# Kernel tuning notes

Hardware: AMD Instinct MI355X
Metric: run time of the kernel (lower is better)

Reference implementation:

```python
import jax, jax.numpy as jnp
import numpy as np

# static config (matches init_kwargs)
NH, NKV, E, K = 16, 4, 8, 2
CAP_FACTOR = 1.25
LN_EPS = 1e-5


def _layer_norm(x, w, b):
    mu = jnp.mean(x, axis=-1, keepdims=True)
    var = jnp.mean(jnp.square(x - mu), axis=-1, keepdims=True)
    return (x - mu) * jax.lax.rsqrt(var + LN_EPS) * w + b


def setup_inputs() -> dict:
    key = jax.random.key(0)
    ks = jax.random.split(key, 6)
    S, B, H, F = 2048, 1, 1024, 2048
    HD = H // NH
    qkv_out = NKV * ((NH // NKV) + 2) * HD  # 1536
    f32 = jnp.float32
    return {
        "hidden_states": jax.random.normal(ks[0], (S, B, H), f32),
        "ln1_weight": jnp.ones((H,), f32),
        "ln1_bias": jnp.zeros((H,), f32),
        "ln2_weight": jnp.ones((H,), f32),
        "ln2_bias": jnp.zeros((H,), f32),
        "qkv_weight": jax.random.normal(ks[1], (qkv_out, H), f32) * 0.02,
        "proj_weight": jax.random.normal(ks[2], (H, H), f32) * 0.02,
        "router_weight": jax.random.normal(ks[3], (H, E), f32) * 0.02,
        "moe_w1": jax.random.normal(ks[4], (E, H, F), f32) * 0.02,
        "moe_w2": jax.random.normal(ks[5], (F and E, F, H), f32)[:E] * 0.02 if False else jax.random.normal(ks[5], (E, F, H), f32) * 0.02,
    }


def reference(hidden_states, ln1_weight, ln1_bias, ln2_weight, ln2_bias,
              qkv_weight, proj_weight, router_weight, moe_w1, moe_w2):
    S, B, H = hidden_states.shape
    HD = H // NH
    q_per_kv = NH // NKV
    # ---- attention block (cp_size=1: all-to-alls are identity) ----
    ln1 = _layer_norm(hidden_states, ln1_weight, ln1_bias)
    qkv = jnp.einsum('sbh,oh->sbo', ln1, qkv_weight)
    qkv = qkv.reshape(S, B, NKV, (q_per_kv + 2) * HD)
    q = qkv[..., : q_per_kv * HD].reshape(S, B, NH, HD)
    k = qkv[..., q_per_kv * HD:(q_per_kv + 1) * HD]          # [S,B,NKV,HD]
    v = qkv[..., (q_per_kv + 1) * HD:]                        # [S,B,NKV,HD]
    qb = jnp.transpose(q, (1, 2, 0, 3)).reshape(B, NKV, q_per_kv, S, HD)
    kb = jnp.transpose(k, (1, 2, 0, 3))                       # [B,NKV,S,HD]
    vb = jnp.transpose(v, (1, 2, 0, 3))
    scale = 1.0 / np.sqrt(HD).astype(np.float32)
    scores = jnp.einsum('bgqsd,bgtd->bgqst', qb, kb) * scale  # [B,NKV,qpk,S,S]
    causal = jnp.tril(jnp.ones((S, S), bool))
    scores = jnp.where(causal, scores, jnp.finfo(scores.dtype).min)
    attn = jax.nn.softmax(scores, axis=-1)
    ao = jnp.einsum('bgqst,bgtd->bgqsd', attn, vb)
    ao = ao.reshape(B, NH, S, HD)
    ao = jnp.transpose(ao, (2, 0, 1, 3)).reshape(S, B, H)
    proj = jnp.einsum('sbh,oh->sbo', ao, proj_weight)
    h1 = hidden_states + proj
    # ---- MoE block (ep_size=1: uniform all-to-all is identity) ----
    ln2 = _layer_norm(h1, ln2_weight, ln2_bias)
    x = ln2.reshape(-1, H)                                    # [N,H]
    N = x.shape[0]
    logits = x @ router_weight                                # linear(x, router_weight.t())
    probs = jax.nn.softmax(logits, axis=-1)
    top_p, top_i = jax.lax.top_k(probs, K)
    top_p = top_p / jnp.sum(top_p, axis=-1, keepdims=True)
    exp_idx = top_i.reshape(-1)                               # [N*K]
    exp_p = top_p.reshape(-1)
    # stable sort by expert id, capacity-padded dispatch
    order = jnp.argsort(exp_idx, stable=True)
    sorted_exp = exp_idx[order]
    counts = jnp.bincount(exp_idx, length=E)
    offsets = jnp.concatenate([jnp.zeros((1,), counts.dtype), jnp.cumsum(counts)[:-1]])
    within = jnp.arange(N * K) - offsets[sorted_exp]
    cap = int(np.ceil(N * K / E * CAP_FACTOR))
    T = E * cap
    valid = within < cap
    dst = jnp.where(valid, sorted_exp * cap + within, T)      # T = out-of-bounds -> dropped
    padded_tokens = jnp.zeros((T, H), x.dtype).at[dst].set(x[order // K], mode='drop')
    padded_probs = jnp.zeros((T,), exp_p.dtype).at[dst].set(exp_p[order], mode='drop')
    padded_tid = jnp.zeros((T,), jnp.int32).at[dst].set((order // K).astype(jnp.int32), mode='drop')
    # grouped expert GEMMs: [E,cap,H] x [E,H,F] -> gelu -> [E,cap,H]
    xt = padded_tokens.reshape(E, cap, H)
    fc1 = jax.nn.gelu(jnp.einsum('ech,ehf->ecf', xt, moe_w1))
    fc2 = jnp.einsum('ecf,efh->ech', fc1, moe_w2).reshape(T, H)
    weighted = fc2 * padded_probs[:, None]                    # pad slots have prob 0
    moe_out = jnp.zeros((N, H), hidden_states.dtype).at[padded_tid].add(weighted)
    return h1 + moe_out.reshape(S, B, H)
```

## Files before the change

kernel.cpp:

```cpp
#include <hip/hip_runtime.h>
#include <hip/hip_bf16.h>
#include <stdint.h>

#define S_LEN 2048
#define HDIM  1024
#define NHEAD 16
#define NKVH  4
#define HEADD 64
#define QKV_O 1536
#define NEXP  8
#define TOPK  2
#define CAP   640
#define TCAP  (NEXP*CAP)
#define FDIM  2048
#define LOG2E 1.44269504088896f
#define NCHUNK 40
#define ATTN_BLOCKS (NCHUNK*NHEAD)
#define TRANSP_BLOCKS 4096

typedef __bf16 bf16x8 __attribute__((ext_vector_type(8)));
typedef float  f32x4  __attribute__((ext_vector_type(4)));
typedef unsigned int u32;
typedef u32 u32x4 __attribute__((ext_vector_type(4)));
typedef u32 u32x2 __attribute__((ext_vector_type(2)));
typedef unsigned short u16;
typedef u16 u16x8 __attribute__((ext_vector_type(8)));

__device__ __forceinline__ void gload16(const __bf16* g, __bf16* l) {
    __builtin_amdgcn_global_load_lds(
        (const __attribute__((address_space(1))) u32*)g,
        (__attribute__((address_space(3))) u32*)l, 16, 0, 0);
}

__device__ __constant__ const signed char c_strip[NCHUNK] =
    {0,1,2,3, 4,4, 5,5, 6,6, 7,7, 8,8,8, 9,9,9, 10,10,10, 11,11,11,
     12,12,12,12, 13,13,13,13, 14,14,14,14, 15,15,15,15};
__device__ __constant__ const signed char c_chunk[NCHUNK] =
    {0,0,0,0, 0,1, 0,1, 0,1, 0,1, 0,1,2, 0,1,2, 0,1,2, 0,1,2,
     0,1,2,3, 0,1,2,3, 0,1,2,3, 0,1,2,3};
__device__ __constant__ const signed char c_cbase[16] = {0,1,2,3,4,6,8,10,12,15,18,21,24,28,32,36};
__device__ __constant__ const signed char c_nch[16]   = {1,1,1,1,2,2,2,2,3,3,3,3,4,4,4,4};

__global__ __launch_bounds__(256)
void prep_kernel(const float* __restrict__ hidden, const float* __restrict__ ln1w,
                 const float* __restrict__ ln1bb, const float* __restrict__ qkvW,
                 const float* __restrict__ projW, __bf16* __restrict__ ln1o,
                 __bf16* __restrict__ projWb, __bf16* __restrict__ qkvWb) {
    const int b = blockIdx.x, tid = threadIdx.x;
    if (b < S_LEN) {
        __shared__ float red[256];
        const float* x = hidden + (size_t)b * HDIM;
        float xr[4];
        #pragma unroll
        for (int j = 0; j < 4; ++j) xr[j] = x[tid + 256*j];
        float s = xr[0] + xr[1] + xr[2] + xr[3];
        red[tid] = s; __syncthreads();
        for (int st = 128; st > 0; st >>= 1) { if (tid < st) red[tid] += red[tid+st]; __syncthreads(); }
        float mu = red[0] / HDIM; __syncthreads();
        float v = 0.f;
        #pragma unroll
        for (int j = 0; j < 4; ++j) { float d = xr[j]-mu; v += d*d; }
        red[tid] = v; __syncthreads();
        for (int st = 128; st > 0; st >>= 1) { if (tid < st) red[tid] += red[tid+st]; __syncthreads(); }
        float rstd = rsqrtf(red[0]/HDIM + 1e-5f);
        #pragma unroll
        for (int j = 0; j < 4; ++j) {
            int i = tid + 256*j;
            ln1o[(size_t)b*HDIM + i] = (__bf16)((xr[j]-mu)*rstd*ln1w[i] + ln1bb[i]);
        }
        return;
    }
    const float* src; __bf16* dst; int i;
    if (b < S_LEN + 768) { src = qkvW; dst = qkvWb; i = (b - S_LEN)*256 + tid; }
    else                 { src = projW; dst = projWb; i = (b - S_LEN - 768)*256 + tid; }
    const float4* s = (const float4*)src + (size_t)i*2;
    float4 a = s[0], b4 = s[1];
    __bf16 tmp[8] = {(__bf16)a.x,(__bf16)a.y,(__bf16)a.z,(__bf16)a.w,
                     (__bf16)b4.x,(__bf16)b4.y,(__bf16)b4.z,(__bf16)b4.w};
    *(u32x4*)(dst + (size_t)i*8) = *(u32x4*)tmp;
}

template<int EPI>
__global__ __launch_bounds__(256)
void gemm_bf16_kernel(const __bf16* __restrict__ A, const __bf16* __restrict__ Bt,
                      const float* __restrict__ R, void* __restrict__ Cout,
                      int N, int K, long sA, long sB, long sC) {
    __shared__ __bf16 As[128*64];
    __shared__ __bf16 Bs[128*64];
    const int e = blockIdx.z;
    A  += (size_t)e * sA;
    Bt += (size_t)e * sB;
    const int m0 = blockIdx.y*128, n0 = blockIdx.x*128;
    const int tid = threadIdx.x;
    const int lane = tid & 63, w = tid >> 6;
    const int lr = lane & 15, lg = lane >> 4;
    const int wr = w >> 1, wc = w & 1;
    const int srow8 = lane >> 3, sg = lane & 7;
    f32x4 acc[4][4] = {};
    for (int k0 = 0; k0 < K; k0 += 64) {
        __syncthreads();
        #pragma unroll
        for (int i = 0; i < 4; ++i) {
            int row = 32*w + 8*i + srow8;
            int src_g = sg ^ (row & 7);
            gload16(A  + (size_t)(m0+row)*K + k0 + src_g*8,
                    (__bf16*)((char*)As + (32*w + 8*i)*128));
            gload16(Bt + (size_t)(n0+row)*K + k0 + src_g*8,
                    (__bf16*)((char*)Bs + (32*w + 8*i)*128));
        }
        __syncthreads();
        #pragma unroll
        for (int ks = 0; ks < 2; ++ks) {
            bf16x8 af[4], bfr[4];
            #pragma unroll
            for (int mi = 0; mi < 4; ++mi) {
                int row = wr*64 + mi*16 + lr;
                af[mi] = *(const bf16x8*)((const char*)As + ((row*128 + (lg+4*ks)*16) ^ ((row&7)<<4)));
            }
            #pragma unroll
            for (int ni = 0; ni < 4; ++ni) {
                int row = wc*64 + ni*16 + lr;
                bfr[ni] = *(const bf16x8*)((const char*)Bs + ((row*128 + (lg+4*ks)*16) ^ ((row&7)<<4)));
            }
            #pragma unroll
            for (int mi = 0; mi < 4; ++mi)
                #pragma unroll
                for (int ni = 0; ni < 4; ++ni)
                    acc[mi][ni] = __builtin_amdgcn_mfma_f32_16x16x32_bf16(af[mi], bfr[ni], acc[mi][ni], 0,0,0);
        }
    }
    #pragma unroll
    for (int mi = 0; mi < 4; ++mi) {
        #pragma unroll
        for (int ni = 0; ni < 4; ++ni) {
            #pragma unroll
            for (int r = 0; r < 4; ++r) {
                int row = m0 + wr*64 + mi*16 + lg*4 + r;
                int col = n0 + wc*64 + ni*16 + lr;
                float v = acc[mi][ni][r];
                if (EPI == 1) v += R[(size_t)row*N + col];
                if (EPI == 2) {
                    float t = 0.7978845608028654f * (v + 0.044715f*v*v*v);
                    v = 0.5f * v * (1.f + tanhf(t));
                }
                if (EPI == 2 || EPI == 3)
                    ((__bf16*)Cout)[(size_t)e*sC + (size_t)row*N + col] = (__bf16)v;
                else
                    ((float*)Cout)[(size_t)e*sC + (size_t)row*N + col] = v;
            }
        }
    }
}

__global__ __launch_bounds__(512)
void attn_transp_kernel(const __bf16* __restrict__ qkv, float* __restrict__ partO,
                        float* __restrict__ partML,
                        const float* __restrict__ w1, const float* __restrict__ w2,
                        __bf16* __restrict__ w1t, __bf16* __restrict__ w2t) {
    __shared__ __attribute__((aligned(16))) char smem[49152];
    const int bid = blockIdx.x;

    if (bid >= ATTN_BLOCKS) {
        const int half = threadIdx.x >> 8, t256 = threadIdx.x & 255;
        float (*t)[65] = (float(*)[65])(smem + half*16640);
        const int tile = (bid - ATTN_BLOCKS)*2 + half;
        const float* src; __bf16* dst; int K, N, n0, k0;
        if (tile < 4096) {
            int e = tile >> 9, rem = tile & 511;
            K = HDIM; N = FDIM; n0 = (rem & 31) * 64; k0 = (rem >> 5) * 64;
            src = w1 + (size_t)e*K*N; dst = w1t + (size_t)e*K*N;
        } else {
            int tt = tile - 4096; int e = tt >> 9, rem = tt & 511;
            K = FDIM; N = HDIM; n0 = (rem & 15) * 64; k0 = (rem >> 4) * 64;
            src = w2 + (size_t)e*K*N; dst = w2t + (size_t)e*K*N;
        }
        const int r = t256 >> 4, c4 = (t256 & 15) * 4;
        #pragma unroll
        for (int i = 0; i < 4; ++i) {
            float4 v = *(const float4*)(src + (size_t)(k0 + r + 16*i)*N + n0 + c4);
            t[r+16*i][c4+0] = v.x; t[r+16*i][c4+1] = v.y;
            t[r+16*i][c4+2] = v.z; t[r+16*i][c4+3] = v.w;
        }
        __syncthreads();
        const int rn = t256 >> 3, kc = (t256 & 7) * 8;
        #pragma unroll
        for (int i = 0; i < 2; ++i) {
            int n = rn + 32*i;
            __bf16 tmp[8];
            #pragma unroll
            for (int j = 0; j < 8; ++j) tmp[j] = (__bf16)t[kc+j][n];
            *(u32x4*)(dst + (size_t)(n0+n)*K + k0 + kc) = *(u32x4*)tmp;
        }
        return;
    }

    __bf16* Kls = (__bf16*)smem;
    __bf16* Vls = (__bf16*)(smem + 16384);
    const int cx = bid % NCHUNK;
    const int h  = bid / NCHUNK;
    const int hg = h >> 2, qi = h & 3;
    const int qb = c_strip[cx];
    const int t0 = 4 * c_chunk[cx];
    const int t1 = min(qb + 1, t0 + 4);
    const int q0 = qb * 128;
    const int tid  = threadIdx.x;
    const int w    = tid >> 6;
    const int lane = tid & 63;
    const int lr   = lane & 15;
    const int lg   = lane >> 4;

    const int krow = tid >> 2, kc = (tid & 3) * 2;
    const int va = tid & 63,  dg  = tid >> 6;
    u32x4 kreg[2]; u16x8 vreg[2];

    const __bf16* kbase = qkv + hg*384 + 256;
    const __bf16* vbase = qkv + hg*384 + 320;

#define ISSUE(T) do { \
        const __bf16* kp = kbase + (size_t)((T)*128 + krow)*QKV_O + kc*8; \
        kreg[0] = *(const u32x4*)(kp); \
        kreg[1] = *(const u32x4*)(kp + 8); \
        const __bf16* vp = vbase + (size_t)((T)*128 + 2*va)*QKV_O + dg*8; \
        vreg[0] = *(const u16x8*)(vp); \
        vreg[1] = *(const u16x8*)(vp + QKV_O); \
    } while(0)

#define COMMIT() do { \
        char* Kb = (char*)Kls; \
        *(u32x4*)(Kb + ((krow*128 + (kc+0)*16) ^ ((krow&7)<<4))) = kreg[0]; \
        *(u32x4*)(Kb + ((krow*128 + (kc+1)*16) ^ ((krow&7)<<4))) = kreg[1]; \
        char* Vb = (char*)Vls; \
        _Pragma("unroll") \
        for (int j = 0; j < 8; ++j) { \
            int d = dg*8 + j; \
            u32 u = ((u32)vreg[1][j] << 16) | vreg[0][j]; \
            *(u32*)(Vb + ((d*256 + va*4) ^ ((d&7)<<4))) = u; \
        } \
    } while(0)

    const int qrow = q0 + w*16 + lr;
    const __bf16* qp = qkv + (size_t)qrow*QKV_O + hg*384 + qi*64;
    bf16x8 qfrag[2];
    #pragma unroll
    for (int ks = 0; ks < 2; ++ks) {
        bf16x8 qr = *(const bf16x8*)(qp + ks*32 + lg*8);
        #pragma unroll
        for (int j = 0; j < 8; ++j) qfrag[ks][j] = (__bf16)((float)qr[j] * 0.125f);
    }
    bf16x8 ones;
    #pragma unroll
    for (int j = 0; j < 8; ++j) ones[j] = (__bf16)1.0f;

    f32x4 oacc[4] = {};
    f32x4 lcol = {};
    float mrow[4] = {-INFINITY,-INFINITY,-INFINITY,-INFINITY};

    ISSUE(t0);
    for (int t = t0; t < t1; ++t) {
        __syncthreads();
        COMMIT();
        if (t+1 < t1) ISSUE(t+1);
        __syncthreads();

        f32x4 sacc[8] = {};
        const char* Kb = (const char*)Kls;
        #pragma unroll
        for (int f = 0; f < 8; ++f) {
            int row = lr + 16*f;
            int swz = (row & 7) << 4;
            #pragma unroll
            for (int ks = 0; ks < 2; ++ks) {
                bf16x8 kf = *(const bf16x8*)(Kb + ((row*128 + (lg*8+32*ks)*2) ^ swz));
                sacc[f] = __builtin_amdgcn_mfma_f32_16x16x32_bf16(qfrag[ks], kf, sacc[f], 0,0,0);
            }
        }
        if (t == qb) {
            #pragma unroll
            for (int f = 0; f < 8; ++f)
                #pragma unroll
                for (int r = 0; r < 4; ++r)
                    if (lr + 16*f > 16*w + 4*lg + r) sacc[f][r] = -INFINITY;
        }
        float tm[4];
        #pragma unroll
        for (int r = 0; r < 4; ++r) {
            float a = fmaxf(fmaxf(sacc[0][r], sacc[1][r]), fmaxf(sacc[2][r], sacc[3][r]));
            float b2 = fmaxf(fmaxf(sacc[4][r], sacc[5][r]), fmaxf(sacc[6][r], sacc[7][r]));
            tm[r] = fmaxf(a, b2);
        }
        #pragma unroll
        for (int msk = 1; msk < 16; msk <<= 1)
            #pragma unroll
            for (int r = 0; r < 4; ++r) tm[r] = fmaxf(tm[r], __shfl_xor(tm[r], msk, 64));
        float corr[4];
        #pragma unroll
        for (int r = 0; r < 4; ++r) {
            float mn = fmaxf(mrow[r], tm[r]);
            corr[r] = exp2f((mrow[r]-mn)*LOG2E);
            mrow[r] = mn;
        }
        #pragma unroll
        for (int f = 0; f < 8; ++f)
            #pragma unroll
            for (int r = 0; r < 4; ++r)
                sacc[f][r] = exp2f((sacc[f][r]-mrow[r])*LOG2E);
        #pragma unroll
        for (int ct = 0; ct < 4; ++ct)
            #pragma unroll
            for (int r = 0; r < 4; ++r) oacc[ct][r] *= corr[r];
        #pragma unroll
        for (int r = 0; r < 4; ++r) lcol[r] *= corr[r];

        char* Pw = smem + 32768 + w*2048;
        const char* Vb = (const char*)Vls;
        #pragma unroll
        for (int half = 0; half < 2; ++half) {
            #pragma unroll
            for (int f = 0; f < 4; ++f)
                #pragma unroll
                for (int r = 0; r < 4; ++r) {
                    int row = 4*lg + r, col = lr + 16*f;
                    *(__bf16*)(Pw + ((row*128 + col*2) ^ ((row&7)<<4))) = (__bf16)sacc[4*half+f][r];
                }
            bf16x8 pa[2];
            #pragma unroll
            for (int ks = 0; ks < 2; ++ks)
                pa[ks] = *(const bf16x8*)(Pw + ((lr*128 + (lg*8+32*ks)*2) ^ ((lr&7)<<4)));
            #pragma unroll
            for (int ks = 0; ks < 2; ++ks)
                lcol = __builtin_amdgcn_mfma_f32_16x16x32_bf16(pa[ks], ones, lcol, 0,0,0);
            #pragma unroll
            for (int ct = 0; ct < 4; ++ct) {
                int row = lr + 16*ct;
                int swz = (row & 7) << 4;
                #pragma unroll
                for (int ks = 0; ks < 2; ++ks) {
                    int gks = 2*half + ks;
                    bf16x8 vf = *(const bf16x8*)(Vb + ((row*256 + (lg*8+32*gks)*2) ^ swz));
                    oacc[ct] = __builtin_amdgcn_mfma_f32_16x16x32_bf16(pa[ks], vf, oacc[ct], 0,0,0);
                }
            }
        }
    }
    const int p = h*NCHUNK + cx;
    float* po = partO + (size_t)p * (128*64);
    #pragma unroll
    for (int ct = 0; ct < 4; ++ct)
        #pragma unroll
        for (int r = 0; r < 4; ++r)
            po[(16*w + 4*lg + r)*64 + 16*ct + lr] = oacc[ct][r];
    if (lr == 0) {
        float* pm = partML + (size_t)p * 256;
        #pragma unroll
        for (int r = 0; r < 4; ++r) {
            pm[(16*w + 4*lg + r)*2    ] = mrow[r];
            pm[(16*w + 4*lg + r)*2 + 1] = lcol[r];
        }
    }
#undef ISSUE
#undef COMMIT
}

__global__ __launch_bounds__(256)
void attn_combine_kernel(const float* __restrict__ partO, const float* __restrict__ partML,
                         __bf16* __restrict__ ao) {
    const int rb = blockIdx.x, h = blockIdx.y;
    const int row0 = rb*8;
    const int qb = row0 >> 7;
    const int nc = c_nch[qb], cb = c_cbase[qb];
    const int tid = threadIdx.x;
    const int rl = tid >> 5, d2 = (tid & 31) * 2;
    const int grow = row0 + rl;
    const int srow = grow & 127;
    const int pbase = h*NCHUNK + cb;
    float mv[4], lv[4];
    float M = -INFINITY;
    for (int c = 0; c < nc; ++c) {
        const float* pm = partML + (size_t)(pbase+c)*256 + srow*2;
        mv[c] = pm[0]; lv[c] = pm[1];
        M = fmaxf(M, mv[c]);
    }
    float L = 0.f, a0 = 0.f, a1 = 0.f;
    for (int c = 0; c < nc; ++c) {
        float wc = exp2f((mv[c]-M)*LOG2E);
        L += wc * lv[c];
        const float* po = partO + (size_t)(pbase+c)*(128*64) + srow*64 + d2;
        a0 += wc * po[0];
        a1 += wc * po[1];
    }
    float inv = 1.f / L;
    __bf16 o2[2] = {(__bf16)(a0*inv), (__bf16)(a1*inv)};
    *(u32*)(ao + (size_t)grow*HDIM + h*64 + d2) = *(u32*)o2;
}

__global__ __launch_bounds__(256)
void ln2_router_kernel(const float* __restrict__ h1, const float* __restrict__ w,
                       const float* __restrict__ b, const float* __restrict__ rw,
                       __bf16* __restrict__ x2b, int* __restrict__ expi,
                       float* __restrict__ expp) {
    const int t = blockIdx.x, tid = threadIdx.x;
    __shared__ float red[256];
    __shared__ float red8[256][8];
    const float* x = h1 + (size_t)t*HDIM;
    float xr[4];
    #pragma unroll
    for (int j = 0; j < 4; ++j) xr[j] = x[tid + 256*j];
    float s = xr[0] + xr[1] + xr[2] + xr[3];
    red[tid] = s; __syncthreads();
    for (int st = 128; st > 0; st >>= 1) { if (tid < st) red[tid] += red[tid+st]; __syncthreads(); }
    float mu = red[0] / HDIM; __syncthreads();
    float v = 0.f;
    #pragma unroll
    for (int j = 0; j < 4; ++j) { float d = xr[j]-mu; v += d*d; }
    red[tid] = v; __syncthreads();
    for (int st = 128; st > 0; st >>= 1) { if (tid < st) red[tid] += red[tid+st]; __syncthreads(); }
    float rstd = rsqrtf(red[0]/HDIM + 1e-5f);
    float part[8] = {};
    #pragma unroll
    for (int j = 0; j < 4; ++j) {
        int i = tid + 256*j;
        float o = (xr[j]-mu)*rstd*w[i] + b[i];
        x2b[(size_t)t*HDIM + i] = (__bf16)o;
        const float* wp = rw + (size_t)i*NEXP;
        #pragma unroll
        for (int e2 = 0; e2 < 8; ++e2) part[e2] += o * wp[e2];
    }
    #pragma unroll
    for (int e2 = 0; e2 < 8; ++e2) red8[tid][e2] = part[e2];
    __syncthreads();
    for (int st = 128; st > 0; st >>= 1) {
        if (tid < st)
            #pragma unroll
            for (int e2 = 0; e2 < 8; ++e2) red8[tid][e2] += red8[tid+st][e2];
        __syncthreads();
    }
    if (tid == 0) {
        float lg[8];
        #pragma unroll
        for (int e2 = 0; e2 < 8; ++e2) lg[e2] = red8[0][e2];
        int i0 = 0;
        for (int e2 = 1; e2 < 8; ++e2) if (lg[e2] > lg[i0]) i0 = e2;
        int i1 = -1;
        for (int e2 = 0; e2 < 8; ++e2) { if (e2 == i0) continue; if (i1 < 0 || lg[e2] > lg[i1]) i1 = e2; }
        float p1 = __expf(lg[i1] - lg[i0]);
        float inv = 1.f / (1.f + p1);
        expi[t*2]   = i0; expi[t*2+1] = i1;
        expp[t*2]   = inv; expp[t*2+1] = p1 * inv;
    }
}

__global__ __launch_bounds__(256)
void dst_fast_kernel(const int* __restrict__ expi, int* __restrict__ dst) {
    __shared__ int hist[256][9];
    const int tid = threadIdx.x;
    int ev[16];
    #pragma unroll
    for (int i = 0; i < 16; i += 4)
        *(int4*)(ev+i) = *(const int4*)(expi + tid*16 + i);
    int cnt[8] = {};
    #pragma unroll
    for (int i = 0; i < 16; ++i)
        #pragma unroll
        for (int e = 0; e < 8; ++e) cnt[e] += (ev[i] == e);
    #pragma unroll
    for (int e = 0; e < 8; ++e) hist[tid][e] = cnt[e];
    __syncthreads();
    const int w = tid >> 6, lane = tid & 63;
    #pragma unroll
    for (int rep = 0; rep < 2; ++rep) {
        int e = w + rep*4;
        int h0 = hist[4*lane+0][e], h1 = hist[4*lane+1][e],
            h2 = hist[4*lane+2][e], h3 = hist[4*lane+3][e];
        int s = h0+h1+h2+h3, inc = s;
        #pragma unroll
        for (int off = 1; off < 64; off <<= 1) {
            int v = __shfl_up(inc, off, 64);
            if (lane >= off) inc += v;
        }
        int excl = inc - s;
        hist[4*lane+0][e] = excl;
        hist[4*lane+1][e] = excl + h0;
        hist[4*lane+2][e] = excl + h0 + h1;
        hist[4*lane+3][e] = excl + h0 + h1 + h2;
    }
    __syncthreads();
    int run[8];
    #pragma unroll
    for (int e = 0; e < 8; ++e) run[e] = hist[tid][e];
    int out[16];
    #pragma unroll
    for (int i = 0; i < 16; ++i) {
        int e = ev[i], within = 0;
        #pragma unroll
        for (int e2 = 0; e2 < 8; ++e2)
            if (e == e2) { within = run[e2]; run[e2]++; }
        out[i] = (within < CAP) ? (e*CAP + within) : -1;
    }
    #pragma unroll
    for (int i = 0; i < 16; i += 4)
        *(int4*)(dst + tid*16 + i) = *(const int4*)(out+i);
}

__global__ void scatter_kernel(const __bf16* __restrict__ x2b, const int* __restrict__ dst,
                               __bf16* __restrict__ xt) {
    int s = blockIdx.x;
    int d = dst[s];
    if (d < 0) return;
    int t = s >> 1;
    int i = threadIdx.x;
    u32x2 v = *(const u32x2*)(x2b + (size_t)t*HDIM + i*4);
    *(u32x2*)(xt + (size_t)d*HDIM + i*4) = v;
}

__global__ void combine_kernel(const float* __restrict__ h1, const float* __restrict__ fc2,
                               const int* __restrict__ dst, const float* __restrict__ expp,
                               float* __restrict__ out) {
    int t = blockIdx.x;
    int d0 = dst[t*2], d1 = dst[t*2+1];
    float p0 = expp[t*2], p1 = expp[t*2+1];
    int i = threadIdx.x * 4;
    float4 v = *(const float4*)(h1 + (size_t)t*HDIM + i);
    if (d0 >= 0) {
        float4 f = *(const float4*)(fc2 + (size_t)d0*HDIM + i);
        v.x += p0*f.x; v.y += p0*f.y; v.z += p0*f.z; v.w += p0*f.w;
    }
    if (d1 >= 0) {
        float4 f = *(const float4*)(fc2 + (size_t)d1*HDIM + i);
        v.x += p1*f.x; v.y += p1*f.y; v.z += p1*f.z; v.w += p1*f.w;
    }
    *(float4*)(out + (size_t)t*HDIM + i) = v;
}

extern "C" void kernel_launch(void* const* d_in, const int* in_sizes, int n_in,
                              void* d_out, int out_size, void* d_ws, size_t ws_size,
                              hipStream_t stream) {
    const float* hidden = (const float*)d_in[0];
    const float* ln1w   = (const float*)d_in[1];
    const float* ln1b_  = (const float*)d_in[2];
    const float* ln2w   = (const float*)d_in[3];
    const float* ln2b_  = (const float*)d_in[4];
    const float* qkvW   = (const float*)d_in[5];
    const float* projW  = (const float*)d_in[6];
    const float* routW  = (const float*)d_in[7];
    const float* w1     = (const float*)d_in[8];
    const float* w2     = (const float*)d_in[9];
    float* out = (float*)d_out;

    char* base = (char*)d_ws;
    __bf16* w1t    = (__bf16*)(base);
    __bf16* w2t    = (__bf16*)(base + 33554432);
    __bf16* ln1b   = (__bf16*)(base);
    __bf16* qkvWb  = (__bf16*)(base + 4194304);
    char* B0 = base + 67108864;
    float*  h1   = (float*)(B0);
    __bf16* xtb  = (__bf16*)(B0 + 8388608);
    __bf16* fc1b = (__bf16*)(B0 + 18874368);
    float*  fc2  = (float*)(B0 + 39845888);
    __bf16* x2b    = (__bf16*)fc2;
    __bf16* qkvb   = (__bf16*)((char*)fc2 + 4194304);
    __bf16* aob    = (__bf16*)((char*)fc2 + 10485760);
    __bf16* projWb = (__bf16*)((char*)fc2 + 14680064);
    int*    expi = (int*)(B0 + 60817408);
    int*    dsts = (int*)(B0 + 60833792);
    float*  expp = (float*)(B0 + 60850176);
    float*  partML = (float*)xtb;
    float*  partO  = (float*)fc1b;

    prep_kernel<<<S_LEN + 768 + 512, 256, 0, stream>>>(
        hidden, ln1w, ln1b_, qkvW, projW, ln1b, projWb, qkvWb);
    gemm_bf16_kernel<3><<<dim3(QKV_O/128, S_LEN/128, 1), 256, 0, stream>>>(
        ln1b, qkvWb, nullptr, qkvb, QKV_O, HDIM, 0, 0, 0);
    attn_transp_kernel<<<ATTN_BLOCKS + TRANSP_BLOCKS, 512, 0, stream>>>(
        qkvb, partO, partML, w1, w2, w1t, w2t);
    attn_combine_kernel<<<dim3(S_LEN/8, NHEAD), 256, 0, stream>>>(partO, partML, aob);
    gemm_bf16_kernel<1><<<dim3(HDIM/128, S_LEN/128, 1), 256, 0, stream>>>(
        aob, projWb, hidden, h1, HDIM, HDIM, 0, 0, 0);
    ln2_router_kernel<<<S_LEN, 256, 0, stream>>>(h1, ln2w, ln2b_, routW, x2b, expi, expp);
    dst_fast_kernel<<<1, 256, 0, stream>>>(expi, dsts);
    scatter_kernel<<<S_LEN*TOPK, 256, 0, stream>>>(x2b, dsts, xtb);
    gemm_bf16_kernel<2><<<dim3(FDIM/128, CAP/128, NEXP), 256, 0, stream>>>(
        xtb, w1t, nullptr, fc1b, FDIM, HDIM,
        (long)CAP*HDIM, (long)FDIM*HDIM, (long)CAP*FDIM);
    gemm_bf16_kernel<0><<<dim3(HDIM/128, CAP/128, NEXP), 256, 0, stream>>>(
        fc1b, w2t, nullptr, fc2, HDIM, FDIM,
        (long)CAP*FDIM, (long)FDIM*HDIM, (long)CAP*HDIM);
    combine_kernel<<<S_LEN, 256, 0, stream>>>(h1, fc2, dsts, expp, out);
}
```

Before: 244.8 us.

## Add 64-row GEMM tile variant and interleave attention blocks among transpose blocks

Adds a 64x128-tile bf16 MFMA GEMM kernel and uses it for the QKV, output-projection and MoE fc2 GEMMs, doubling the block count so the 256 CUs are better filled. Separately, the fused attention/weight-transpose launch now places one attention block in every seven block IDs instead of putting all attention blocks first. This spreads the long attention blocks across the dispatch order so they overlap with the short transpose tiles. Smaller tiles lower data reuse per block, and the fixed interleave mapping assumes the block-count ratio stays the same.

```diff
diff --git a/kernel.cpp b/kernel.cpp
--- a/kernel.cpp
+++ b/kernel.cpp
@@ -152,6 +152,82 @@
     }
 }
 
+template<int EPI>
+__global__ __launch_bounds__(256)
+void gemm64_bf16_kernel(const __bf16* __restrict__ A, const __bf16* __restrict__ Bt,
+                        const float* __restrict__ R, void* __restrict__ Cout,
+                        int N, int K, long sA, long sB, long sC) {
+    __shared__ __bf16 As[64*64];
+    __shared__ __bf16 Bs[128*64];
+    const int e = blockIdx.z;
+    A  += (size_t)e * sA;
+    Bt += (size_t)e * sB;
+    const int m0 = blockIdx.y*64, n0 = blockIdx.x*128;
+    const int tid = threadIdx.x;
+    const int lane = tid & 63, w = tid >> 6;
+    const int lr = lane & 15, lg = lane >> 4;
+    const int srow8 = lane >> 3, sg = lane & 7;
+    f32x4 acc[4][2] = {};
+    for (int k0 = 0; k0 < K; k0 += 64) {
+        __syncthreads();
+        #pragma unroll
+        for (int i = 0; i < 2; ++i) {
+            int row = 16*w + 8*i + srow8;
+            int src_g = sg ^ (row & 7);
+            gload16(A + (size_t)(m0+row)*K + k0 + src_g*8,
+                    (__bf16*)((char*)As + (16*w + 8*i)*128));
+        }
+        #pragma unroll
+        for (int i = 0; i < 4; ++i) {
+            int row = 32*w + 8*i + srow8;
+            int src_g = sg ^ (row & 7);
+            gload16(Bt + (size_t)(n0+row)*K + k0 + src_g*8,
+                    (__bf16*)((char*)Bs + (32*w + 8*i)*128));
+        }
+        __syncthreads();
+        #pragma unroll
+        for (int ks = 0; ks < 2; ++ks) {
+            bf16x8 af[4], bfr[2];
+            #pragma unroll
+            for (int mi = 0; mi < 4; ++mi) {
+                int row = mi*16 + lr;
+                af[mi] = *(const bf16x8*)((const char*)As + ((row*128 + (lg+4*ks)*16) ^ ((row&7)<<4)));
+            }
+            #pragma unroll
+            for (int ni = 0; ni < 2; ++ni) {
+                int row = w*32 + ni*16 + lr;
+                bfr[ni] = *(const bf16x8*)((const char*)Bs + ((row*128 + (lg+4*ks)*16) ^ ((row&7)<<4)));
+            }
+            #pragma unroll
+            for (int mi = 0; mi < 4; ++mi)
+                #pragma unroll
+                for (int ni = 0; ni < 2; ++ni)
+                    acc[mi][ni] = __builtin_amdgcn_mfma_f32_16x16x32_bf16(af[mi], bfr[ni], acc[mi][ni], 0,0,0);
+        }
+    }
+    #pragma unroll
+    for (int mi = 0; mi < 4; ++mi) {
+        #pragma unroll
+        for (int ni = 0; ni < 2; ++ni) {
+            #pragma unroll
+            for (int r = 0; r < 4; ++r) {
+                int row = m0 + mi*16 + lg*4 + r;
+                int col = n0 + w*32 + ni*16 + lr;
+                float v = acc[mi][ni][r];
+                if (EPI == 1) v += R[(size_t)row*N + col];
+                if (EPI == 2) {
+                    float t = 0.7978845608028654f * (v + 0.044715f*v*v*v);
+                    v = 0.5f * v * (1.f + tanhf(t));
+                }
+                if (EPI == 2 || EPI == 3)
+                    ((__bf16*)Cout)[(size_t)e*sC + (size_t)row*N + col] = (__bf16)v;
+                else
+                    ((float*)Cout)[(size_t)e*sC + (size_t)row*N + col] = v;
+            }
+        }
+    }
+}
+
 __global__ __launch_bounds__(512)
 void attn_transp_kernel(const __bf16* __restrict__ qkv, float* __restrict__ partO,
                         float* __restrict__ partML,
@@ -159,11 +235,13 @@
                         __bf16* __restrict__ w1t, __bf16* __restrict__ w2t) {
     __shared__ __attribute__((aligned(16))) char smem[49152];
     const int bid = blockIdx.x;
-
-    if (bid >= ATTN_BLOCKS) {
+    const bool is_attn = ((bid % 7) == 3) && (bid / 7 < ATTN_BLOCKS);
+
+    if (!is_attn) {
+        const int tb = bid - min(ATTN_BLOCKS, (bid + 3) / 7);
         const int half = threadIdx.x >> 8, t256 = threadIdx.x & 255;
         float (*t)[65] = (float(*)[65])(smem + half*16640);
-        const int tile = (bid - ATTN_BLOCKS)*2 + half;
+        const int tile = tb*2 + half;
         const float* src; __bf16* dst; int K, N, n0, k0;
         if (tile < 4096) {
             int e = tile >> 9, rem = tile & 511;
@@ -196,8 +274,9 @@
 
     __bf16* Kls = (__bf16*)smem;
     __bf16* Vls = (__bf16*)(smem + 16384);
-    const int cx = bid % NCHUNK;
-    const int h  = bid / NCHUNK;
+    const int a = bid / 7;
+    const int cx = a % NCHUNK;
+    const int h  = a / NCHUNK;
     const int hg = h >> 2, qi = h & 3;
     const int qb = c_strip[cx];
     const int t0 = 4 * c_chunk[cx];
@@ -284,9 +363,9 @@
         float tm[4];
         #pragma unroll
         for (int r = 0; r < 4; ++r) {
-            float a = fmaxf(fmaxf(sacc[0][r], sacc[1][r]), fmaxf(sacc[2][r], sacc[3][r]));
+            float a2 = fmaxf(fmaxf(sacc[0][r], sacc[1][r]), fmaxf(sacc[2][r], sacc[3][r]));
             float b2 = fmaxf(fmaxf(sacc[4][r], sacc[5][r]), fmaxf(sacc[6][r], sacc[7][r]));
-            tm[r] = fmaxf(a, b2);
+            tm[r] = fmaxf(a2, b2);
         }
         #pragma unroll
         for (int msk = 1; msk < 16; msk <<= 1)
@@ -568,12 +647,12 @@
 
     prep_kernel<<<S_LEN + 768 + 512, 256, 0, stream>>>(
         hidden, ln1w, ln1b_, qkvW, projW, ln1b, projWb, qkvWb);
-    gemm_bf16_kernel<3><<<dim3(QKV_O/128, S_LEN/128, 1), 256, 0, stream>>>(
+    gemm64_bf16_kernel<3><<<dim3(QKV_O/128, S_LEN/64, 1), 256, 0, stream>>>(
         ln1b, qkvWb, nullptr, qkvb, QKV_O, HDIM, 0, 0, 0);
     attn_transp_kernel<<<ATTN_BLOCKS + TRANSP_BLOCKS, 512, 0, stream>>>(
         qkvb, partO, partML, w1, w2, w1t, w2t);
     attn_combine_kernel<<<dim3(S_LEN/8, NHEAD), 256, 0, stream>>>(partO, partML, aob);
-    gemm_bf16_kernel<1><<<dim3(HDIM/128, S_LEN/128, 1), 256, 0, stream>>>(
+    gemm64_bf16_kernel<1><<<dim3(HDIM/128, S_LEN/64, 1), 256, 0, stream>>>(
         aob, projWb, hidden, h1, HDIM, HDIM, 0, 0, 0);
     ln2_router_kernel<<<S_LEN, 256, 0, stream>>>(h1, ln2w, ln2b_, routW, x2b, expi, expp);
     dst_fast_kernel<<<1, 256, 0, stream>>>(expi, dsts);
@@ -581,7 +660,7 @@
     gemm_bf16_kernel<2><<<dim3(FDIM/128, CAP/128, NEXP), 256, 0, stream>>>(
         xtb, w1t, nullptr, fc1b, FDIM, HDIM,
         (long)CAP*HDIM, (long)FDIM*HDIM, (long)CAP*FDIM);
-    gemm_bf16_kernel<0><<<dim3(HDIM/128, CAP/128, NEXP), 256, 0, stream>>>(
+    gemm64_bf16_kernel<0><<<dim3(HDIM/128, CAP/64, NEXP), 256, 0, stream>>>(
         fc1b, w2t, nullptr, fc2, HDIM, FDIM,
         (long)CAP*FDIM, (long)FDIM*HDIM, (long)CAP*HDIM);
     combine_kernel<<<S_LEN, 256, 0, stream>>>(h1, fc2, dsts, expp, out);
```

New measurement: 229.3 us (median of 2 runs). 6.3% less time.
